# Kernel optimization log

Hardware: AMD Instinct MI355X
Metric: run time of the kernel (lower is better)

Reference implementation:

```python
import jax, jax.numpy as jnp
import numpy as np

N, E, F, H, G = 50000, 1600000, 128, 128, 64
EPS = 1e-5  # BatchNorm eps


def setup_inputs() -> dict:
    key = jax.random.key(0)
    ks = jax.random.split(key, 16)
    x = jax.random.normal(ks[0], (N, F), dtype=jnp.float32)
    edge_index = jax.random.randint(ks[1], (2, E), 0, N, dtype=jnp.int64)
    batch = jnp.sort(jax.random.randint(ks[2], (N,), 0, G, dtype=jnp.int64))
    inp = {
        'x': x, 'edge_index': edge_index, 'batch': batch,
        'W1': jax.random.normal(ks[3], (F, H), dtype=jnp.float32) / np.sqrt(F),
        'b1': jnp.zeros((H,), jnp.float32),
        'bn1_gamma': jax.random.uniform(ks[4], (H,), jnp.float32, 0.5, 1.5),
        'bn1_beta': jax.random.normal(ks[5], (H,), jnp.float32) * 0.1,
        'bn1_mean': jax.random.normal(ks[6], (H,), jnp.float32) * 0.1,
        'bn1_var': jax.random.uniform(ks[7], (H,), jnp.float32, 0.5, 1.5),
        'W2': jax.random.normal(ks[8], (H, H), dtype=jnp.float32) / np.sqrt(H),
        'b2': jnp.zeros((H,), jnp.float32),
        'bn2_gamma': jax.random.uniform(ks[9], (H,), jnp.float32, 0.5, 1.5),
        'bn2_beta': jax.random.normal(ks[10], (H,), jnp.float32) * 0.1,
        'bn2_mean': jax.random.normal(ks[11], (H,), jnp.float32) * 0.1,
        'bn2_var': jax.random.uniform(ks[12], (H,), jnp.float32, 0.5, 1.5),
        'att_w': jax.random.normal(ks[13], (H, 1), dtype=jnp.float32) / np.sqrt(H),
        'cls_w': jax.random.normal(ks[14], (1, H), dtype=jnp.float32) / np.sqrt(H),
        'cls_b': jnp.zeros((1,), jnp.float32),
    }
    return inp


def gcn_conv(h, W, b, src, dst, n):
    # PyG GCNConv: linear, add self-loops, symmetric D^{-1/2}(A+I)D^{-1/2} aggregation, bias.
    hw = h @ W                                   # [n, H]
    loops = jnp.arange(n, dtype=src.dtype)
    s = jnp.concatenate([src, loops])
    d = jnp.concatenate([dst, loops])
    deg = jax.ops.segment_sum(jnp.ones_like(d, dtype=hw.dtype), d, num_segments=n)
    dis = jnp.where(deg > 0, jax.lax.rsqrt(deg), 0.0)
    norm = dis[s] * dis[d]                       # [E+n]
    msgs = hw[s] * norm[:, None]                 # gather + scale (memory-bound)
    return jax.ops.segment_sum(msgs, d, num_segments=n) + b


def batch_norm(h, gamma, beta, mean, var):
    return (h - mean) * gamma * jax.lax.rsqrt(var + EPS) + beta


def reference(x, edge_index, batch, W1, b1, bn1_gamma, bn1_beta, bn1_mean, bn1_var,
              W2, b2, bn2_gamma, bn2_beta, bn2_mean, bn2_var, att_w, cls_w, cls_b):
    n = x.shape[0]
    src, dst = edge_index[0], edge_index[1]
    # eval mode: dropout and edge-dropout are no-ops; BN uses running stats
    h = gcn_conv(x, W1, b1, src, dst, n)
    h = jax.nn.relu(batch_norm(h, bn1_gamma, bn1_beta, bn1_mean, bn1_var))
    h = gcn_conv(h, W2, b2, src, dst, n)
    h = jax.nn.relu(batch_norm(h, bn2_gamma, bn2_beta, bn2_mean, bn2_var))
    att = jax.nn.sigmoid(h @ att_w)              # [n, 1]
    g = jax.ops.segment_sum(h * att, batch, num_segments=G)  # [G, H]
    logits = g @ cls_w.T + cls_b                 # [G, 1]
    return logits, att
```

## Files before the change

### kernel.cpp

```cpp
#include <hip/hip_runtime.h>
#include <math.h>

#define NN 50000
#define HID 128
#define NG 64
#define BN_EPS 1e-5f

typedef __attribute__((ext_vector_type(8))) short short8;
typedef __attribute__((ext_vector_type(4))) float f32x4;

__device__ inline unsigned pack_bf2(float a, float b) {
    union { float f; unsigned u; } ua, ub;
    ua.f = a; ub.f = b;
    unsigned x = ua.u, y = ub.u;
    x += 0x7fffu + ((x >> 16) & 1u);
    y += 0x7fffu + ((y >> 16) & 1u);
    return (x >> 16) | (y & 0xffff0000u);
}
__device__ inline unsigned short bf16_1(float x) {
    union { float f; unsigned u; } v;
    v.f = x;
    unsigned r = v.u + 0x7fffu + ((v.u >> 16) & 1u);
    return (unsigned short)(r >> 16);
}
__device__ inline float2 unpack_bf2(unsigned v) {
    union { unsigned u; float f; } a, b;
    a.u = v << 16;
    b.u = v & 0xffff0000u;
    return make_float2(a.f, b.f);
}

#define NBKT 256
#define ETILE 8192
#define CAP   8192

__global__ __launch_bounds__(256) void k_distribute(const int* __restrict__ src,
                                                    const int* __restrict__ dst,
                                                    int* __restrict__ bcurP,
                                                    unsigned* __restrict__ bpacked,
                                                    const float* __restrict__ W1,
                                                    const float* __restrict__ W2,
                                                    unsigned short* __restrict__ wt1,
                                                    unsigned short* __restrict__ wt2,
                                                    int etiles, int E, int K) {
    if ((int)blockIdx.x >= etiles) {
        int b2 = blockIdx.x - etiles;
        int k = b2 & 127;
        const float* W = (b2 < 128) ? W1 : W2;
        unsigned short* wt = (b2 < 128) ? wt1 : wt2;
        int c = threadIdx.x;
        if (c < 128) wt[c * 128 + k] = bf16_1(W[k * 128 + c]);
        return;
    }
    __shared__ int h[NBKT];
    int t = threadIdx.x;
    h[t] = 0;
    __syncthreads();
    int base = blockIdx.x * ETILE;
    for (int i = 0; i < ETILE / 256; ++i) {
        int e = base + i * 256 + t;
        if (e < E) atomicAdd(&h[dst[e] / K], 1);
    }
    __syncthreads();
    int c = h[t];
    int my = (c > 0) ? atomicAdd(&bcurP[t * 16], c) : 0;
    __syncthreads();
    h[t] = my;
    __syncthreads();
    for (int i = 0; i < ETILE / 256; ++i) {
        int e = base + i * 256 + t;
        if (e < E) {
            int d = dst[e];
            int bkt = d / K;
            int p = atomicAdd(&h[bkt], 1);
            bpacked[(size_t)bkt * CAP + p] = ((unsigned)d << 16) | (unsigned)src[e];
        }
    }
}

__global__ __launch_bounds__(256) void k_bucket_csr(const unsigned* __restrict__ bpacked,
                                                    const int* __restrict__ bcurP,
                                                    int* __restrict__ row_ptr,
                                                    int* __restrict__ degA,
                                                    float* __restrict__ dis,
                                                    int* __restrict__ col_idx,
                                                    const float* __restrict__ cls_b,
                                                    float* __restrict__ logits,
                                                    int n, int K) {
    __shared__ int cnt[NBKT];
    __shared__ int sA[NBKT];
    __shared__ int cur[NBKT];
    int t = threadIdx.x;
    int b = blockIdx.x;
    if (b == 0 && t < NG) logits[t] = cls_b[0];
    int node0 = b * K;
    int nn = n - node0;
    if (nn > K) nn = K;
    if (nn < 0) nn = 0;
    int e0 = b * CAP;
    int e1 = e0 + bcurP[b * 16];
    cnt[t] = 0;
    __syncthreads();
    for (int e = e0 + t; e < e1; e += 256) {
        int ld = (int)(bpacked[e] >> 16) - node0;
        atomicAdd(&cnt[ld], 1);
    }
    __syncthreads();
    int c = cnt[t];
    sA[t] = c;
    __syncthreads();
    for (int off = 1; off < NBKT; off <<= 1) {
        int v = (t >= off) ? sA[t - off] : 0;
        __syncthreads();
        sA[t] += v;
        __syncthreads();
    }
    int rp = e0 + sA[t] - c;
    cur[t] = rp;
    if (t < nn) {
        row_ptr[node0 + t] = rp;
        degA[node0 + t] = c;
        dis[node0 + t] = rsqrtf((float)(c + 1));
    }
    __syncthreads();
    for (int e = e0 + t; e < e1; e += 256) {
        unsigned v = bpacked[e];
        int ld = (int)(v >> 16) - node0;
        int p = atomicAdd(&cur[ld], 1);
        col_idx[p] = (int)(v & 0xFFFFu);
    }
}


#define ASTR 136

__global__ __launch_bounds__(256) void k_gemm_mfma(const float* __restrict__ in,
                                                   const unsigned short* __restrict__ wt,
                                                   const float* __restrict__ dis,
                                                   unsigned short* __restrict__ outb, int n) {
    __shared__ unsigned short A[64][ASTR];
    int t = threadIdx.x;
    int row0 = blockIdx.x * 64;

    #pragma unroll
    for (int i = 0; i < 8; ++i) {
        int idx = t + i * 256;
        int r = idx >> 5;
        int c4 = (idx & 31) * 4;
        float4 v = make_float4(0.f, 0.f, 0.f, 0.f);
        if (row0 + r < n) v = *(const float4*)&in[(size_t)(row0 + r) * 128 + c4];
        uint2 p;
        p.x = pack_bf2(v.x, v.y);
        p.y = pack_bf2(v.z, v.w);
        *(uint2*)&A[r][c4] = p;
    }
    __syncthreads();

    int lane = t & 63;
    int wave = t >> 6;
    int m = lane & 15;
    int quad = lane >> 4;
    int r0 = wave * 16;

    short8 a[4];
    #pragma unroll
    for (int kt = 0; kt < 4; ++kt)
        a[kt] = *(const short8*)&A[r0 + m][kt * 32 + quad * 8];

    f32x4 acc[8];
    #pragma unroll
    for (int ct = 0; ct < 8; ++ct) acc[ct] = (f32x4){0.f, 0.f, 0.f, 0.f};

    short8 bcur[4], bnxt[4];
    {
        const unsigned short* wb = &wt[(size_t)m * 128 + quad * 8];
        #pragma unroll
        for (int kt = 0; kt < 4; ++kt) bcur[kt] = *(const short8*)(wb + kt * 32);
    }
    #pragma unroll
    for (int ct = 0; ct < 8; ++ct) {
        if (ct < 7) {
            const unsigned short* wb = &wt[(size_t)((ct + 1) * 16 + m) * 128 + quad * 8];
            #pragma unroll
            for (int kt = 0; kt < 4; ++kt) bnxt[kt] = *(const short8*)(wb + kt * 32);
        }
        #pragma unroll
        for (int kt = 0; kt < 4; ++kt)
            acc[ct] = __builtin_amdgcn_mfma_f32_16x16x32_bf16(a[kt], bcur[kt], acc[ct], 0, 0, 0);
        #pragma unroll
        for (int kt = 0; kt < 4; ++kt) bcur[kt] = bnxt[kt];
    }

    int gr = row0 + r0 + quad * 4;
    float ds[4];
    #pragma unroll
    for (int reg = 0; reg < 4; ++reg)
        ds[reg] = (gr + reg < n) ? dis[gr + reg] : 0.f;

    __syncthreads();
    #pragma unroll
    for (int ct = 0; ct < 8; ++ct) {
        int col = ct * 16 + m;
        #pragma unroll
        for (int reg = 0; reg < 4; ++reg)
            A[r0 + quad * 4 + reg][col] = bf16_1(acc[ct][reg] * ds[reg]);
    }
    __syncthreads();
    #pragma unroll
    for (int i = 0; i < 4; ++i) {
        int idx = t + i * 256;
        int r = idx >> 4;
        int c8 = (idx & 15) * 8;
        int grow = row0 + r;
        if (grow < n)
            *(uint4*)&outb[(size_t)grow * 128 + c8] = *(const uint4*)&A[r][c8];
    }
}


__device__ inline void gather4wide(const unsigned short* __restrict__ hwsb,
                                   const int* __restrict__ col_idx,
                                   int e0, int deg, int md,
                                   int sl, int part, bool active,
                                   float* acc8) {
    int cidx = (active && sl < deg) ? col_idx[e0 + sl] : 0;
    for (int it0 = 0; it0 < md; it0 += 16) {
        int nx = it0 + 16;
        int cidx_next = (active && (nx + sl) < deg && nx < md) ? col_idx[e0 + nx + sl] : 0;
        uint4 vv[16];
        #pragma unroll
        for (int j = 0; j < 16; ++j) {
            int s = __shfl(cidx, (part << 4) + j);
            vv[j] = (it0 + j < deg)
                        ? *(const uint4*)(hwsb + ((size_t)s << 7) + (sl << 3))
                        : make_uint4(0, 0, 0, 0);
        }
        #pragma unroll
        for (int j = 0; j < 16; ++j) {
            const unsigned* w = (const unsigned*)&vv[j];
            #pragma unroll
            for (int i2 = 0; i2 < 4; ++i2) {
                float2 f = unpack_bf2(w[i2]);
                acc8[2 * i2]     += f.x;
                acc8[2 * i2 + 1] += f.y;
            }
        }
        cidx = cidx_next;
    }
}


__global__ __launch_bounds__(256) void k_agg1_gemm2(const unsigned short* __restrict__ hwsb1,
                                                    const int* __restrict__ row_ptr,
                                                    const int* __restrict__ degA,
                                                    const int* __restrict__ col_idx,
                                                    const float* __restrict__ dis,
                                                    const float* __restrict__ bias,
                                                    const float* __restrict__ gamma,
                                                    const float* __restrict__ beta,
                                                    const float* __restrict__ mean,
                                                    const float* __restrict__ var,
                                                    const unsigned short* __restrict__ wt2,
                                                    unsigned short* __restrict__ hwsb2, int n) {
    __shared__ unsigned short H1[16][ASTR];
    __shared__ unsigned short C2[16][ASTR];
    int t = threadIdx.x;
    int wave = t >> 6, lane = t & 63;
    int sl = lane & 15, part = lane >> 4;
    int d = blockIdx.x * 16 + wave * 4 + part;
    bool active = (d < n);
    int e0 = 0, deg = 0;
    if (active) {
        e0 = row_ptr[d];
        deg = degA[d];
    }
    int md = deg;
    md = max(md, __shfl_xor(md, 16));
    md = max(md, __shfl_xor(md, 32));

    float acc8[8] = {0, 0, 0, 0, 0, 0, 0, 0};
    gather4wide(hwsb1, col_idx, e0, deg, md, sl, part, active, acc8);

    unsigned outw[4] = {0, 0, 0, 0};
    if (active) {
        uint4 v = *(const uint4*)(hwsb1 + ((size_t)d << 7) + (sl << 3));
        const unsigned* w = (const unsigned*)&v;
        #pragma unroll
        for (int i2 = 0; i2 < 4; ++i2) {
            float2 f = unpack_bf2(w[i2]);
            acc8[2 * i2]     += f.x;
            acc8[2 * i2 + 1] += f.y;
        }
        float dd = dis[d];
        int f0 = sl << 3;
        #pragma unroll
        for (int i2 = 0; i2 < 4; ++i2) {
            int f = f0 + 2 * i2;
            float2 bv = *(const float2*)&bias[f];
            float2 gm = *(const float2*)&gamma[f];
            float2 bt = *(const float2*)&beta[f];
            float2 mn = *(const float2*)&mean[f];
            float2 vr = *(const float2*)&var[f];
            float vx = acc8[2 * i2] * dd + bv.x;
            float vy = acc8[2 * i2 + 1] * dd + bv.y;
            float sx = gm.x * rsqrtf(vr.x + BN_EPS);
            float sy = gm.y * rsqrtf(vr.y + BN_EPS);
            float rx = fmaxf((vx - mn.x) * sx + bt.x, 0.f);
            float ry = fmaxf((vy - mn.y) * sy + bt.y, 0.f);
            outw[i2] = pack_bf2(rx, ry);
        }
    }
    int local = wave * 4 + part;
    *(uint4*)&H1[local][sl << 3] = *(uint4*)outw;
    __syncthreads();

    int m = sl;
    int quad = part;
    short8 a2[4];
    #pragma unroll
    for (int kt = 0; kt < 4; ++kt)
        a2[kt] = *(const short8*)&H1[m][kt * 32 + quad * 8];

    f32x4 acc2[2];
    acc2[0] = (f32x4){0.f, 0.f, 0.f, 0.f};
    acc2[1] = (f32x4){0.f, 0.f, 0.f, 0.f};
    #pragma unroll
    for (int i = 0; i < 2; ++i) {
        int ct = wave * 2 + i;
        const unsigned short* wb = &wt2[(size_t)(ct * 16 + m) * 128 + quad * 8];
        #pragma unroll
        for (int kt = 0; kt < 4; ++kt) {
            short8 b = *(const short8*)(wb + kt * 32);
            acc2[i] = __builtin_amdgcn_mfma_f32_16x16x32_bf16(a2[kt], b, acc2[i], 0, 0, 0);
        }
    }
    int gr = blockIdx.x * 16 + quad * 4;
    float ds2[4];
    #pragma unroll
    for (int reg = 0; reg < 4; ++reg)
        ds2[reg] = (gr + reg < n) ? dis[gr + reg] : 0.f;
    #pragma unroll
    for (int i = 0; i < 2; ++i) {
        int col = (wave * 2 + i) * 16 + m;
        #pragma unroll
        for (int reg = 0; reg < 4; ++reg)
            C2[quad * 4 + reg][col] = bf16_1(acc2[i][reg] * ds2[reg]);
    }
    __syncthreads();
    {
        int r = t >> 4;
        int c8 = (t & 15) * 8;
        int grow = blockIdx.x * 16 + r;
        if (grow < n)
            *(uint4*)&hwsb2[(size_t)grow * 128 + c8] = *(const uint4*)&C2[r][c8];
    }
}


__global__ __launch_bounds__(256) void k_agg2_att_logit(const unsigned short* __restrict__ hwsb,
                                                        const int* __restrict__ row_ptr,
                                                        const int* __restrict__ degA,
                                                        const int* __restrict__ col_idx,
                                                        const float* __restrict__ dis,
                                                        const float* __restrict__ bias,
                                                        const float* __restrict__ gamma,
                                                        const float* __restrict__ beta,
                                                        const float* __restrict__ mean,
                                                        const float* __restrict__ var,
                                                        const int* __restrict__ batch,
                                                        const float* __restrict__ att_w,
                                                        const float* __restrict__ cls_w,
                                                        float* __restrict__ att_out,
                                                        float* __restrict__ logits, int n) {
    __shared__ int   sg[16];
    __shared__ float sv[16];
    int t = threadIdx.x;
    int wave = t >> 6, lane = t & 63;
    int sl = lane & 15, part = lane >> 4;
    int d = blockIdx.x * 16 + wave * 4 + part;
    bool active = (d < n);
    int e0 = 0, deg = 0;
    if (active) {
        e0 = row_ptr[d];
        deg = degA[d];
    }
    int md = deg;
    md = max(md, __shfl_xor(md, 16));
    md = max(md, __shfl_xor(md, 32));

    float acc8[8] = {0, 0, 0, 0, 0, 0, 0, 0};
    gather4wide(hwsb, col_idx, e0, deg, md, sl, part, active, acc8);

    int g = -1;
    float contrib = 0.f;
    float p = 0.f, q = 0.f;
    if (active) {
        uint4 v = *(const uint4*)(hwsb + ((size_t)d << 7) + (sl << 3));
        const unsigned* w = (const unsigned*)&v;
        #pragma unroll
        for (int i2 = 0; i2 < 4; ++i2) {
            float2 f = unpack_bf2(w[i2]);
            acc8[2 * i2]     += f.x;
            acc8[2 * i2 + 1] += f.y;
        }
        float dd = dis[d];
        int f0 = sl << 3;
        #pragma unroll
        for (int i2 = 0; i2 < 4; ++i2) {
            int f = f0 + 2 * i2;
            float2 bv = *(const float2*)&bias[f];
            float2 gm = *(const float2*)&gamma[f];
            float2 bt = *(const float2*)&beta[f];
            float2 mn = *(const float2*)&mean[f];
            float2 vr = *(const float2*)&var[f];
            float vx = acc8[2 * i2] * dd + bv.x;
            float vy = acc8[2 * i2 + 1] * dd + bv.y;
            float sx = gm.x * rsqrtf(vr.x + BN_EPS);
            float sy = gm.y * rsqrtf(vr.y + BN_EPS);
            float rx = fmaxf((vx - mn.x) * sx + bt.x, 0.f);
            float ry = fmaxf((vy - mn.y) * sy + bt.y, 0.f);
            float2 aw = *(const float2*)&att_w[f];
            float2 cw = *(const float2*)&cls_w[f];
            p += rx * aw.x + ry * aw.y;
            q += rx * cw.x + ry * cw.y;
        }
    }
    #pragma unroll
    for (int off = 1; off < 16; off <<= 1) {
        p += __shfl_xor(p, off);
        q += __shfl_xor(q, off);
    }
    if (active) {
        float a = 1.f / (1.f + expf(-p));
        if (sl == 0) att_out[d] = a;
        g = batch[d];
        contrib = a * q;
    }
    if (sl == 0) {
        sg[wave * 4 + part] = g;
        sv[wave * 4 + part] = contrib;
    }
    __syncthreads();
    if (t == 0) {
        int cur = -1;
        float acc = 0.f;
        #pragma unroll
        for (int i = 0; i < 16; ++i) {
            int gi = sg[i];
            if (gi < 0) continue;
            if (gi != cur) {
                if (cur >= 0) atomicAdd(&logits[cur], acc);
                cur = gi;
                acc = 0.f;
            }
            acc += sv[i];
        }
        if (cur >= 0) atomicAdd(&logits[cur], acc);
    }
}


extern "C" void kernel_launch(void* const* d_in, const int* in_sizes, int n_in,
                              void* d_out, int out_size, void* d_ws, size_t ws_size,
                              hipStream_t stream) {
    const float* x   = (const float*)d_in[0];
    const int*   ei  = (const int*)d_in[1];
    const int*   bat = (const int*)d_in[2];
    const float* W1  = (const float*)d_in[3];
    const float* b1  = (const float*)d_in[4];
    const float* g1  = (const float*)d_in[5];
    const float* bt1 = (const float*)d_in[6];
    const float* mn1 = (const float*)d_in[7];
    const float* vr1 = (const float*)d_in[8];
    const float* W2  = (const float*)d_in[9];
    const float* b2  = (const float*)d_in[10];
    const float* g2  = (const float*)d_in[11];
    const float* bt2 = (const float*)d_in[12];
    const float* mn2 = (const float*)d_in[13];
    const float* vr2 = (const float*)d_in[14];
    const float* attw = (const float*)d_in[15];
    const float* clsw = (const float*)d_in[16];
    const float* clsb = (const float*)d_in[17];

    int E = in_sizes[1] / 2;
    int n = in_sizes[2];
    const int* src = ei;
    const int* dst = ei + E;
    int K = (n + NBKT - 1) / NBKT;

    char* ws = (char*)d_ws;
    auto alloc = [&](size_t bytes) {
        void* p = (void*)ws;
        ws += (bytes + 255) & ~(size_t)255;
        return p;
    };
    int*            bcurP   = (int*)alloc(NBKT * 16 * 4);
    unsigned*       bpacked = (unsigned*)alloc((size_t)NBKT * CAP * 4);
    int*            row_ptr = (int*)alloc((size_t)n * 4);
    int*            degA    = (int*)alloc((size_t)n * 4);
    int*            col_idx = (int*)alloc((size_t)NBKT * CAP * 4);
    float*          dis     = (float*)alloc((size_t)n * 4);
    unsigned short* hwsb1   = (unsigned short*)alloc((size_t)n * 128 * 2);
    unsigned short* hwsb2   = (unsigned short*)alloc((size_t)n * 128 * 2);
    unsigned short* wt1     = (unsigned short*)alloc(128 * 128 * 2);
    unsigned short* wt2     = (unsigned short*)alloc(128 * 128 * 2);

    float* out = (float*)d_out;
    int etiles = (E + ETILE - 1) / ETILE;
    int gb = (n + 63) / 64;
    int ab = (n + 15) / 16;

    hipMemsetAsync(bcurP, 0, NBKT * 16 * 4, stream);
    k_distribute<<<etiles + 256, 256, 0, stream>>>(src, dst, bcurP, bpacked,
                                                   W1, W2, wt1, wt2, etiles, E, K);
    k_bucket_csr<<<NBKT, 256, 0, stream>>>(bpacked, bcurP, row_ptr, degA, dis,
                                           col_idx, clsb, out, n, K);

    k_gemm_mfma<<<gb, 256, 0, stream>>>(x, wt1, dis, hwsb1, n);
    k_agg1_gemm2<<<ab, 256, 0, stream>>>(hwsb1, row_ptr, degA, col_idx, dis,
                                         b1, g1, bt1, mn1, vr1, wt2, hwsb2, n);
    k_agg2_att_logit<<<ab, 256, 0, stream>>>(hwsb2, row_ptr, degA, col_idx, dis,
                                             b2, g2, bt2, mn2, vr2, bat, attw, clsw,
                                             out + NG, out, n);
}
```

Baseline: 293.7 us.

## Merge first GEMM into CSR build kernel and scale by source norm at gather

The first-layer X·W1 GEMM no longer needs the degree normalisation, so it runs as extra blocks inside the CSR-building kernel instead of as a separate launch afterwards. The per-source D^{-1/2} factor is now applied during the layer-1 gather by loading dis[src] alongside each column index. The memset and weight transpose move into a small prep kernel, which removes one launch and lets the GEMM overlap the bucket-to-CSR work. In exchange, the gather does an extra random dis load per edge, and the merged kernel's larger shared memory footprint can lower occupancy for the CSR blocks.

```diff
diff --git a/kernel.cpp b/kernel.cpp
--- a/kernel.cpp
+++ b/kernel.cpp
@@ -33,25 +33,34 @@
 #define NBKT 256
 #define ETILE 8192
 #define CAP   8192
+#define ASTR 136
+
+__global__ __launch_bounds__(128) void k_prep0(const float* __restrict__ W1,
+                                               const float* __restrict__ W2,
+                                               unsigned short* __restrict__ wt1,
+                                               unsigned short* __restrict__ wt2,
+                                               int* __restrict__ bcurP,
+                                               const float* __restrict__ cls_b,
+                                               float* __restrict__ logits) {
+    int b = blockIdx.x;
+    int t = threadIdx.x;
+    if (b < 256) {
+        int k = b & 127;
+        const float* W = (b < 128) ? W1 : W2;
+        unsigned short* wt = (b < 128) ? wt1 : wt2;
+        wt[t * 128 + k] = bf16_1(W[k * 128 + t]);
+    } else {
+        #pragma unroll
+        for (int i = 0; i < 32; ++i) bcurP[t * 32 + i] = 0;
+        if (t < NG) logits[t] = cls_b[0];
+    }
+}
 
 __global__ __launch_bounds__(256) void k_distribute(const int* __restrict__ src,
                                                     const int* __restrict__ dst,
                                                     int* __restrict__ bcurP,
                                                     unsigned* __restrict__ bpacked,
-                                                    const float* __restrict__ W1,
-                                                    const float* __restrict__ W2,
-                                                    unsigned short* __restrict__ wt1,
-                                                    unsigned short* __restrict__ wt2,
-                                                    int etiles, int E, int K) {
-    if ((int)blockIdx.x >= etiles) {
-        int b2 = blockIdx.x - etiles;
-        int k = b2 & 127;
-        const float* W = (b2 < 128) ? W1 : W2;
-        unsigned short* wt = (b2 < 128) ? wt1 : wt2;
-        int c = threadIdx.x;
-        if (c < 128) wt[c * 128 + k] = bf16_1(W[k * 128 + c]);
-        return;
-    }
+                                                    int E, int K) {
     __shared__ int h[NBKT];
     int t = threadIdx.x;
     h[t] = 0;
@@ -78,21 +87,90 @@
     }
 }
 
-__global__ __launch_bounds__(256) void k_bucket_csr(const unsigned* __restrict__ bpacked,
-                                                    const int* __restrict__ bcurP,
-                                                    int* __restrict__ row_ptr,
-                                                    int* __restrict__ degA,
-                                                    float* __restrict__ dis,
-                                                    int* __restrict__ col_idx,
-                                                    const float* __restrict__ cls_b,
-                                                    float* __restrict__ logits,
-                                                    int n, int K) {
+__global__ __launch_bounds__(256) void k_csr_gemm1(const unsigned* __restrict__ bpacked,
+                                                   const int* __restrict__ bcurP,
+                                                   int* __restrict__ row_ptr,
+                                                   int* __restrict__ degA,
+                                                   float* __restrict__ dis,
+                                                   int* __restrict__ col_idx,
+                                                   const float* __restrict__ x,
+                                                   const unsigned short* __restrict__ wt1,
+                                                   unsigned short* __restrict__ zb,
+                                                   int n, int K) {
+    __shared__ unsigned short A[64][ASTR];
     __shared__ int cnt[NBKT];
     __shared__ int sA[NBKT];
     __shared__ int cur[NBKT];
     int t = threadIdx.x;
     int b = blockIdx.x;
-    if (b == 0 && t < NG) logits[t] = cls_b[0];
+
+    if (b >= NBKT) {
+        int row0 = (b - NBKT) * 64;
+        #pragma unroll
+        for (int i = 0; i < 8; ++i) {
+            int idx = t + i * 256;
+            int r = idx >> 5;
+            int c4 = (idx & 31) * 4;
+            float4 v = make_float4(0.f, 0.f, 0.f, 0.f);
+            if (row0 + r < n) v = *(const float4*)&x[(size_t)(row0 + r) * 128 + c4];
+            uint2 p;
+            p.x = pack_bf2(v.x, v.y);
+            p.y = pack_bf2(v.z, v.w);
+            *(uint2*)&A[r][c4] = p;
+        }
+        __syncthreads();
+        int lane = t & 63;
+        int wave = t >> 6;
+        int m = lane & 15;
+        int quad = lane >> 4;
+        int r0 = wave * 16;
+        short8 a[4];
+        #pragma unroll
+        for (int kt = 0; kt < 4; ++kt)
+            a[kt] = *(const short8*)&A[r0 + m][kt * 32 + quad * 8];
+        f32x4 acc[8];
+        #pragma unroll
+        for (int ct = 0; ct < 8; ++ct) acc[ct] = (f32x4){0.f, 0.f, 0.f, 0.f};
+        short8 bcur[4], bnxt[4];
+        {
+            const unsigned short* wb = &wt1[(size_t)m * 128 + quad * 8];
+            #pragma unroll
+            for (int kt = 0; kt < 4; ++kt) bcur[kt] = *(const short8*)(wb + kt * 32);
+        }
+        #pragma unroll
+        for (int ct = 0; ct < 8; ++ct) {
+            if (ct < 7) {
+                const unsigned short* wb = &wt1[(size_t)((ct + 1) * 16 + m) * 128 + quad * 8];
+                #pragma unroll
+                for (int kt = 0; kt < 4; ++kt) bnxt[kt] = *(const short8*)(wb + kt * 32);
+            }
+            #pragma unroll
+            for (int kt = 0; kt < 4; ++kt)
+                acc[ct] = __builtin_amdgcn_mfma_f32_16x16x32_bf16(a[kt], bcur[kt], acc[ct], 0, 0, 0);
+            #pragma unroll
+            for (int kt = 0; kt < 4; ++kt) bcur[kt] = bnxt[kt];
+        }
+        __syncthreads();
+        #pragma unroll
+        for (int ct = 0; ct < 8; ++ct) {
+            int col = ct * 16 + m;
+            #pragma unroll
+            for (int reg = 0; reg < 4; ++reg)
+                A[r0 + quad * 4 + reg][col] = bf16_1(acc[ct][reg]);
+        }
+        __syncthreads();
+        #pragma unroll
+        for (int i = 0; i < 4; ++i) {
+            int idx = t + i * 256;
+            int r = idx >> 4;
+            int c8 = (idx & 15) * 8;
+            int grow = row0 + r;
+            if (grow < n)
+                *(uint4*)&zb[(size_t)grow * 128 + c8] = *(const uint4*)&A[r][c8];
+        }
+        return;
+    }
+
     int node0 = b * K;
     int nn = n - node0;
     if (nn > K) nn = K;
@@ -128,92 +206,6 @@
         int ld = (int)(v >> 16) - node0;
         int p = atomicAdd(&cur[ld], 1);
         col_idx[p] = (int)(v & 0xFFFFu);
-    }
-}
-
-
-#define ASTR 136
-
-__global__ __launch_bounds__(256) void k_gemm_mfma(const float* __restrict__ in,
-                                                   const unsigned short* __restrict__ wt,
-                                                   const float* __restrict__ dis,
-                                                   unsigned short* __restrict__ outb, int n) {
-    __shared__ unsigned short A[64][ASTR];
-    int t = threadIdx.x;
-    int row0 = blockIdx.x * 64;
-
-    #pragma unroll
-    for (int i = 0; i < 8; ++i) {
-        int idx = t + i * 256;
-        int r = idx >> 5;
-        int c4 = (idx & 31) * 4;
-        float4 v = make_float4(0.f, 0.f, 0.f, 0.f);
-        if (row0 + r < n) v = *(const float4*)&in[(size_t)(row0 + r) * 128 + c4];
-        uint2 p;
-        p.x = pack_bf2(v.x, v.y);
-        p.y = pack_bf2(v.z, v.w);
-        *(uint2*)&A[r][c4] = p;
-    }
-    __syncthreads();
-
-    int lane = t & 63;
-    int wave = t >> 6;
-    int m = lane & 15;
-    int quad = lane >> 4;
-    int r0 = wave * 16;
-
-    short8 a[4];
-    #pragma unroll
-    for (int kt = 0; kt < 4; ++kt)
-        a[kt] = *(const short8*)&A[r0 + m][kt * 32 + quad * 8];
-
-    f32x4 acc[8];
-    #pragma unroll
-    for (int ct = 0; ct < 8; ++ct) acc[ct] = (f32x4){0.f, 0.f, 0.f, 0.f};
-
-    short8 bcur[4], bnxt[4];
-    {
-        const unsigned short* wb = &wt[(size_t)m * 128 + quad * 8];
-        #pragma unroll
-        for (int kt = 0; kt < 4; ++kt) bcur[kt] = *(const short8*)(wb + kt * 32);
-    }
-    #pragma unroll
-    for (int ct = 0; ct < 8; ++ct) {
-        if (ct < 7) {
-            const unsigned short* wb = &wt[(size_t)((ct + 1) * 16 + m) * 128 + quad * 8];
-            #pragma unroll
-            for (int kt = 0; kt < 4; ++kt) bnxt[kt] = *(const short8*)(wb + kt * 32);
-        }
-        #pragma unroll
-        for (int kt = 0; kt < 4; ++kt)
-            acc[ct] = __builtin_amdgcn_mfma_f32_16x16x32_bf16(a[kt], bcur[kt], acc[ct], 0, 0, 0);
-        #pragma unroll
-        for (int kt = 0; kt < 4; ++kt) bcur[kt] = bnxt[kt];
-    }
-
-    int gr = row0 + r0 + quad * 4;
-    float ds[4];
-    #pragma unroll
-    for (int reg = 0; reg < 4; ++reg)
-        ds[reg] = (gr + reg < n) ? dis[gr + reg] : 0.f;
-
-    __syncthreads();
-    #pragma unroll
-    for (int ct = 0; ct < 8; ++ct) {
-        int col = ct * 16 + m;
-        #pragma unroll
-        for (int reg = 0; reg < 4; ++reg)
-            A[r0 + quad * 4 + reg][col] = bf16_1(acc[ct][reg] * ds[reg]);
-    }
-    __syncthreads();
-    #pragma unroll
-    for (int i = 0; i < 4; ++i) {
-        int idx = t + i * 256;
-        int r = idx >> 4;
-        int c8 = (idx & 15) * 8;
-        int grow = row0 + r;
-        if (grow < n)
-            *(uint4*)&outb[(size_t)grow * 128 + c8] = *(const uint4*)&A[r][c8];
     }
 }
 
@@ -249,8 +241,46 @@
     }
 }
 
-
-__global__ __launch_bounds__(256) void k_agg1_gemm2(const unsigned short* __restrict__ hwsb1,
+__device__ inline void gather4wide_scaled(const unsigned short* __restrict__ zb,
+                                          const int* __restrict__ col_idx,
+                                          const float* __restrict__ dis,
+                                          int e0, int deg, int md,
+                                          int sl, int part, bool active,
+                                          float* acc8) {
+    int cidx = (active && sl < deg) ? col_idx[e0 + sl] : 0;
+    float cdis = (active && sl < deg) ? dis[cidx] : 0.f;
+    for (int it0 = 0; it0 < md; it0 += 16) {
+        int nx = it0 + 16;
+        bool okn = (active && (nx + sl) < deg && nx < md);
+        int cidx_next = okn ? col_idx[e0 + nx + sl] : 0;
+        float cdis_next = okn ? dis[cidx_next] : 0.f;
+        uint4 vv[16];
+        float dsj[16];
+        #pragma unroll
+        for (int j = 0; j < 16; ++j) {
+            int s = __shfl(cidx, (part << 4) + j);
+            dsj[j] = __shfl(cdis, (part << 4) + j);
+            vv[j] = (it0 + j < deg)
+                        ? *(const uint4*)(zb + ((size_t)s << 7) + (sl << 3))
+                        : make_uint4(0, 0, 0, 0);
+        }
+        #pragma unroll
+        for (int j = 0; j < 16; ++j) {
+            const unsigned* w = (const unsigned*)&vv[j];
+            #pragma unroll
+            for (int i2 = 0; i2 < 4; ++i2) {
+                float2 f = unpack_bf2(w[i2]);
+                acc8[2 * i2]     = fmaf(f.x, dsj[j], acc8[2 * i2]);
+                acc8[2 * i2 + 1] = fmaf(f.y, dsj[j], acc8[2 * i2 + 1]);
+            }
+        }
+        cidx = cidx_next;
+        cdis = cdis_next;
+    }
+}
+
+
+__global__ __launch_bounds__(256) void k_agg1_gemm2(const unsigned short* __restrict__ zb,
                                                     const int* __restrict__ row_ptr,
                                                     const int* __restrict__ degA,
                                                     const int* __restrict__ col_idx,
@@ -279,19 +309,19 @@
     md = max(md, __shfl_xor(md, 32));
 
     float acc8[8] = {0, 0, 0, 0, 0, 0, 0, 0};
-    gather4wide(hwsb1, col_idx, e0, deg, md, sl, part, active, acc8);
+    gather4wide_scaled(zb, col_idx, dis, e0, deg, md, sl, part, active, acc8);
 
     unsigned outw[4] = {0, 0, 0, 0};
     if (active) {
-        uint4 v = *(const uint4*)(hwsb1 + ((size_t)d << 7) + (sl << 3));
+        float dd = dis[d];
+        uint4 v = *(const uint4*)(zb + ((size_t)d << 7) + (sl << 3));
         const unsigned* w = (const unsigned*)&v;
         #pragma unroll
         for (int i2 = 0; i2 < 4; ++i2) {
             float2 f = unpack_bf2(w[i2]);
-            acc8[2 * i2]     += f.x;
-            acc8[2 * i2 + 1] += f.y;
-        }
-        float dd = dis[d];
+            acc8[2 * i2]     = fmaf(f.x, dd, acc8[2 * i2]);
+            acc8[2 * i2 + 1] = fmaf(f.y, dd, acc8[2 * i2 + 1]);
+        }
         int f0 = sl << 3;
         #pragma unroll
         for (int i2 = 0; i2 < 4; ++i2) {
@@ -500,7 +530,7 @@
     int*            degA    = (int*)alloc((size_t)n * 4);
     int*            col_idx = (int*)alloc((size_t)NBKT * CAP * 4);
     float*          dis     = (float*)alloc((size_t)n * 4);
-    unsigned short* hwsb1   = (unsigned short*)alloc((size_t)n * 128 * 2);
+    unsigned short* zb      = (unsigned short*)alloc((size_t)n * 128 * 2);
     unsigned short* hwsb2   = (unsigned short*)alloc((size_t)n * 128 * 2);
     unsigned short* wt1     = (unsigned short*)alloc(128 * 128 * 2);
     unsigned short* wt2     = (unsigned short*)alloc(128 * 128 * 2);
@@ -510,14 +540,11 @@
     int gb = (n + 63) / 64;
     int ab = (n + 15) / 16;
 
-    hipMemsetAsync(bcurP, 0, NBKT * 16 * 4, stream);
-    k_distribute<<<etiles + 256, 256, 0, stream>>>(src, dst, bcurP, bpacked,
-                                                   W1, W2, wt1, wt2, etiles, E, K);
-    k_bucket_csr<<<NBKT, 256, 0, stream>>>(bpacked, bcurP, row_ptr, degA, dis,
-                                           col_idx, clsb, out, n, K);
-
-    k_gemm_mfma<<<gb, 256, 0, stream>>>(x, wt1, dis, hwsb1, n);
-    k_agg1_gemm2<<<ab, 256, 0, stream>>>(hwsb1, row_ptr, degA, col_idx, dis,
+    k_prep0<<<257, 128, 0, stream>>>(W1, W2, wt1, wt2, bcurP, clsb, out);
+    k_distribute<<<etiles, 256, 0, stream>>>(src, dst, bcurP, bpacked, E, K);
+    k_csr_gemm1<<<NBKT + gb, 256, 0, stream>>>(bpacked, bcurP, row_ptr, degA, dis,
+                                               col_idx, x, wt1, zb, n, K);
+    k_agg1_gemm2<<<ab, 256, 0, stream>>>(zb, row_ptr, degA, col_idx, dis,
                                          b1, g1, bt1, mn1, vr1, wt2, hwsb2, n);
     k_agg2_att_logit<<<ab, 256, 0, stream>>>(hwsb2, row_ptr, degA, col_idx, dis,
                                              b2, g2, bt2, mn2, vr2, bat, attw, clsw,
```

Measured after the change: 287.6 us. 2.1% less time.
